# Optimization experiments

Measured on AMD Instinct MI355X. Metric: run time of the kernel, lower is better.

## Reference

```python
import jax, jax.numpy as jnp
import numpy as np

B, S, H, P = 16, 8192, 512, 32

def setup_inputs() -> dict:
    key = jax.random.key(0)
    k1, k2 = jax.random.split(key)
    birnn_outputs = jax.random.normal(k1, (B, S, H), dtype=jnp.float32)
    self_attn = jax.random.normal(k2, (P, H), dtype=jnp.float32)
    return {"birnn_outputs": birnn_outputs, "self_attn": self_attn}

def reference(birnn_outputs, self_attn):
    # scores: [B, P, S] = probes [P,H] x birnn_outputs^T [B,H,S]
    scores = jnp.einsum('ph,bsh->bps', self_attn, birnn_outputs)
    attn = jax.nn.softmax(scores, axis=-1)  # softmax over seq_len
    # context: [B, P, H]
    ctx = jnp.einsum('bps,bsh->bph', attn, birnn_outputs)
    return ctx.reshape(ctx.shape[0], -1)  # [B, P*H]
```

## Files before the change

kernel.cpp:

```cpp
#include <hip/hip_runtime.h>
#include <hip/hip_bf16.h>

#define BB 16
#define SS 8192
#define HH 512
#define PP 32

typedef __attribute__((ext_vector_type(8))) short short8;
typedef __attribute__((ext_vector_type(4))) float f32x4;

__device__ inline unsigned short bf16_hi_trunc(float x) {
  union { float f; unsigned u; } v; v.f = x;
  return (unsigned short)(v.u >> 16);
}
__device__ inline unsigned short bf16_rne(float x) {
  union { float f; unsigned u; } v; v.f = x;
  unsigned r = v.u + 0x7FFFu + ((v.u >> 16) & 1u);
  return (unsigned short)(r >> 16);
}
__device__ inline float from_hi(unsigned short h) {
  union { unsigned u; float f; } v; v.u = ((unsigned)h) << 16;
  return v.f;
}
__device__ inline f32x4 max4(f32x4 a, f32x4 b) {
  f32x4 r; r.x = fmaxf(a.x, b.x); r.y = fmaxf(a.y, b.y);
  r.z = fmaxf(a.z, b.z); r.w = fmaxf(a.w, b.w); return r;
}
__device__ inline f32x4 exp4(f32x4 a) {
  f32x4 r; r.x = __expf(a.x); r.y = __expf(a.y);
  r.z = __expf(a.z); r.w = __expf(a.w); return r;
}
__device__ inline f32x4 fma_b(float a, f32x4 b, f32x4 c) {
  c.x = fmaf(a, b.x, c.x); c.y = fmaf(a, b.y, c.y);
  c.z = fmaf(a, b.z, c.z); c.w = fmaf(a, b.w, c.w); return c;
}
__device__ inline void cvt8(const float* xv, short8& bh, short8& bl) {
#pragma unroll
  for (int j = 0; j < 8; ++j) {
    unsigned short h = bf16_hi_trunc(xv[j]);
    bh[j] = (short)h;
    bl[j] = (short)bf16_rne(xv[j] - from_hi(h));
  }
}

__global__ void k_prep(const float* __restrict__ probes,
                       short* __restrict__ Ph, short* __restrict__ Pl) {
  int t = threadIdx.x;
  for (int q = t; q < 2048; q += 256) {
    int lane = q & 63, kcg = (q >> 6) & 15, nt = q >> 10;
    int p = nt * 16 + (lane & 15);
    int h0 = kcg * 32 + (lane >> 4) * 8;
#pragma unroll
    for (int j = 0; j < 8; ++j) {
      float f = probes[p * HH + h0 + j];
      unsigned short h = bf16_hi_trunc(f);
      Ph[q * 8 + j] = (short)h;
      Pl[q * 8 + j] = (short)bf16_rne(f - from_hi(h));
    }
  }
}

__global__ __launch_bounds__(256) void k_scores4(
    const float* __restrict__ x, const short* __restrict__ Ph,
    const short* __restrict__ Pl, float* __restrict__ scoresT) {
  const int t = threadIdx.x;
  const int lane = t & 63, w = t >> 6;
  const int b = blockIdx.y;
  const int stile = blockIdx.x;

  f32x4 acc[2];
  acc[0] = (f32x4){0.f, 0.f, 0.f, 0.f};
  acc[1] = (f32x4){0.f, 0.f, 0.f, 0.f};

  const int srow = stile * 64 + w * 16 + (lane & 15);
  const float* xr = x + ((size_t)b * SS + srow) * HH + (lane >> 4) * 8;

#pragma unroll 2
  for (int kcg = 0; kcg < 16; ++kcg) {
    f32x4 xa = *(const f32x4*)(xr + kcg * 32);
    f32x4 xc = *(const f32x4*)(xr + kcg * 32 + 4);
    float xv[8] = {xa.x, xa.y, xa.z, xa.w, xc.x, xc.y, xc.z, xc.w};
    short8 xh, xl;
    cvt8(xv, xh, xl);
    short8 ph0 = *(const short8*)(Ph + ((size_t)(kcg * 64 + lane)) * 8);
    short8 pl0 = *(const short8*)(Pl + ((size_t)(kcg * 64 + lane)) * 8);
    short8 ph1 = *(const short8*)(Ph + ((size_t)((16 + kcg) * 64 + lane)) * 8);
    short8 pl1 = *(const short8*)(Pl + ((size_t)((16 + kcg) * 64 + lane)) * 8);
    acc[0] = __builtin_amdgcn_mfma_f32_16x16x32_bf16(xh, ph0, acc[0], 0, 0, 0);
    acc[0] = __builtin_amdgcn_mfma_f32_16x16x32_bf16(xh, pl0, acc[0], 0, 0, 0);
    acc[0] = __builtin_amdgcn_mfma_f32_16x16x32_bf16(xl, ph0, acc[0], 0, 0, 0);
    acc[1] = __builtin_amdgcn_mfma_f32_16x16x32_bf16(xh, ph1, acc[1], 0, 0, 0);
    acc[1] = __builtin_amdgcn_mfma_f32_16x16x32_bf16(xh, pl1, acc[1], 0, 0, 0);
    acc[1] = __builtin_amdgcn_mfma_f32_16x16x32_bf16(xl, ph1, acc[1], 0, 0, 0);
  }

#pragma unroll
  for (int nt = 0; nt < 2; ++nt)
#pragma unroll
    for (int r = 0; r < 4; ++r) {
      int s = stile * 64 + w * 16 + (lane >> 4) * 4 + r;
      int p = nt * 16 + (lane & 15);
      scoresT[((size_t)b * SS + s) * PP + p] = acc[nt][r];
    }
}

__global__ __launch_bounds__(256) void k_stats_a(
    const float* __restrict__ scoresT, float* __restrict__ pm,
    float* __restrict__ pl_) {
  const int blk = blockIdx.x;
  const int b = blk >> 5, sr = blk & 31;
  const int t = threadIdx.x;
  const int p4 = t & 7, sg = t >> 3;
  const f32x4* base = (const f32x4*)(scoresT + ((size_t)b * SS + sr * 256) * PP);

  f32x4 m4 = (f32x4){-1e30f, -1e30f, -1e30f, -1e30f};
  f32x4 l4 = (f32x4){0.f, 0.f, 0.f, 0.f};
#pragma unroll
  for (int i = 0; i < 8; ++i) {
    int s = sg + 32 * i;
    f32x4 v = base[s * 8 + p4];
    f32x4 nm = max4(m4, v);
    l4 = l4 * exp4(m4 - nm) + exp4(v - nm);
    m4 = nm;
  }
  __shared__ f32x4 sm[32][8], sl[32][8];
  sm[sg][p4] = m4;
  sl[sg][p4] = l4;
  __syncthreads();
  if (t < 8) {
    f32x4 M = sm[0][t], L = sl[0][t];
#pragma unroll
    for (int i = 1; i < 32; ++i) {
      f32x4 m2 = sm[i][t], l2 = sl[i][t];
      f32x4 nm = max4(M, m2);
      L = L * exp4(M - nm) + l2 * exp4(m2 - nm);
      M = nm;
    }
    *(f32x4*)&pm[blk * PP + t * 4] = M;
    *(f32x4*)&pl_[blk * PP + t * 4] = L;
  }
}

__global__ __launch_bounds__(256) void k_stats_b(
    const float* __restrict__ pm, const float* __restrict__ pl_,
    float* __restrict__ Mv, float* __restrict__ invl) {
  int i = blockIdx.x * 256 + threadIdx.x;
  if (i >= BB * PP) return;
  int b = i >> 5, p = i & 31;
  float M = -1e30f, L = 0.f;
#pragma unroll
  for (int sr = 0; sr < 32; ++sr) {
    float m2 = pm[(b * 32 + sr) * PP + p], l2 = pl_[(b * 32 + sr) * PP + p];
    float nm = fmaxf(M, m2);
    L = L * __expf(M - nm) + l2 * __expf(m2 - nm);
    M = nm;
  }
  Mv[i] = M;
  invl[i] = 1.0f / L;
}

__global__ __launch_bounds__(256) void k_ctx4(
    const float* __restrict__ x, const float* __restrict__ scoresT,
    const float* __restrict__ Mv, const float* __restrict__ invl,
    float* __restrict__ part) {
  __shared__ float wl[256 * PP];
  const int t = threadIdx.x;
  const int lane = t & 63, w = t >> 6;
  const int sc = blockIdx.x, hh = blockIdx.y, b = blockIdx.z;

  const int pbase = (4 * t) & 31;
  f32x4 mv = *(const f32x4*)(Mv + b * PP + pbase);
  f32x4 il = *(const f32x4*)(invl + b * PP + pbase);
  const f32x4* src = (const f32x4*)(scoresT + ((size_t)b * SS + sc * 256) * PP);
#pragma unroll
  for (int it = 0; it < 8; ++it) {
    f32x4 v = src[t + 256 * it];
    f32x4 e;
    e.x = __expf(v.x - mv.x) * il.x;
    e.y = __expf(v.y - mv.y) * il.y;
    e.z = __expf(v.z - mv.z) * il.z;
    e.w = __expf(v.w - mv.w) * il.w;
    *(f32x4*)&wl[(t + 256 * it) * 4] = e;
  }
  __syncthreads();

  const float* xrow = x + ((size_t)b * SS + sc * 256) * HH + hh * 256 + lane * 4;
  const f32x4* wj = (const f32x4*)wl;

  f32x4 acc[8];
#pragma unroll
  for (int k = 0; k < 8; ++k) acc[k] = (f32x4){0.f, 0.f, 0.f, 0.f};

  for (int jo = 0; jo < 256; jo += 8) {
    f32x4 xv[8];
#pragma unroll
    for (int u = 0; u < 8; ++u)
      xv[u] = *(const f32x4*)(xrow + (size_t)(jo + u) * HH);
#pragma unroll
    for (int u = 0; u < 8; ++u) {
      int j = jo + u;
      f32x4 w0 = wj[j * 8 + w * 2];
      f32x4 w1 = wj[j * 8 + w * 2 + 1];
      acc[0] = fma_b(w0.x, xv[u], acc[0]);
      acc[1] = fma_b(w0.y, xv[u], acc[1]);
      acc[2] = fma_b(w0.z, xv[u], acc[2]);
      acc[3] = fma_b(w0.w, xv[u], acc[3]);
      acc[4] = fma_b(w1.x, xv[u], acc[4]);
      acc[5] = fma_b(w1.y, xv[u], acc[5]);
      acc[6] = fma_b(w1.z, xv[u], acc[6]);
      acc[7] = fma_b(w1.w, xv[u], acc[7]);
    }
  }

#pragma unroll
  for (int pi = 0; pi < 8; ++pi) {
    int p = w * 8 + pi;
    *(f32x4*)(part + (((size_t)sc * BB + b) * PP + p) * HH + hh * 256 + lane * 4) =
        acc[pi];
  }
}

__global__ __launch_bounds__(256) void k_reduce(const float* __restrict__ part,
                                               float* __restrict__ out) {
  int i = blockIdx.x * 256 + threadIdx.x;
  float s = 0.f;
#pragma unroll
  for (int c = 0; c < 32; ++c) s += part[(size_t)c * (BB * PP * HH) + i];
  out[i] = s;
}

extern "C" void kernel_launch(void* const* d_in, const int* in_sizes, int n_in,
                              void* d_out, int out_size, void* d_ws, size_t ws_size,
                              hipStream_t stream) {
  const float* x = (const float*)d_in[0];
  const float* probes = (const float*)d_in[1];
  float* out = (float*)d_out;

  float* scoresT = (float*)d_ws;
  float* part = scoresT + (size_t)BB * SS * PP;
  float* Mv = part + (size_t)32 * BB * PP * HH;
  float* invl = Mv + BB * PP;
  float* pm = invl + BB * PP;
  float* pl_ = pm + 512 * PP;
  short* Ph = (short*)(pl_ + 512 * PP);
  short* Pl = Ph + PP * HH;

  k_prep<<<1, 256, 0, stream>>>(probes, Ph, Pl);
  k_scores4<<<dim3(SS / 64, BB), 256, 0, stream>>>(x, Ph, Pl, scoresT);
  k_stats_a<<<dim3(512), 256, 0, stream>>>(scoresT, pm, pl_);
  k_stats_b<<<dim3(2), 256, 0, stream>>>(pm, pl_, Mv, invl);
  k_ctx4<<<dim3(32, 2, BB), 256, 0, stream>>>(x, scoresT, Mv, invl, part);
  k_reduce<<<dim3(BB * PP * HH / 256), 256, 0, stream>>>(part, out);
}
```

Before: 471.8 us.

## Fuse scores, local softmax and context into one flash-style chunk kernel

```diff
diff --git a/kernel.cpp b/kernel.cpp
--- a/kernel.cpp
+++ b/kernel.cpp
@@ -5,6 +5,8 @@
 #define SS 8192
 #define HH 512
 #define PP 32
+#define NC 32
+#define CH 256
 
 typedef __attribute__((ext_vector_type(8))) short short8;
 typedef __attribute__((ext_vector_type(4))) float f32x4;
@@ -60,173 +62,164 @@
   }
 }
 
-__global__ __launch_bounds__(256) void k_scores4(
+__global__ __launch_bounds__(512, 4) void k_fused(
     const float* __restrict__ x, const short* __restrict__ Ph,
-    const short* __restrict__ Pl, float* __restrict__ scoresT) {
+    const short* __restrict__ Pl, float* __restrict__ pm,
+    float* __restrict__ pl_, float* __restrict__ part) {
+  __shared__ float sc_[CH][36];
+  __shared__ f32x4 sm[64][8];
+  __shared__ f32x4 sl[64][8];
+  __shared__ f32x4 mS4[8];
+
   const int t = threadIdx.x;
   const int lane = t & 63, w = t >> 6;
+  const int scnk = blockIdx.x;
   const int b = blockIdx.y;
-  const int stile = blockIdx.x;
-
-  f32x4 acc[2];
-  acc[0] = (f32x4){0.f, 0.f, 0.f, 0.f};
-  acc[1] = (f32x4){0.f, 0.f, 0.f, 0.f};
-
-  const int srow = stile * 64 + w * 16 + (lane & 15);
-  const float* xr = x + ((size_t)b * SS + srow) * HH + (lane >> 4) * 8;
-
+  const size_t xbase = ((size_t)b * SS + (size_t)scnk * CH) * HH;
+
+#pragma unroll
+  for (int tile = 0; tile < CH / 128; ++tile) {
+    f32x4 acc0 = (f32x4){0.f, 0.f, 0.f, 0.f};
+    f32x4 acc1 = (f32x4){0.f, 0.f, 0.f, 0.f};
+    const int rl = tile * 128 + w * 16 + (lane & 15);
+    const float* xr = x + xbase + (size_t)rl * HH + (lane >> 4) * 8;
 #pragma unroll 2
-  for (int kcg = 0; kcg < 16; ++kcg) {
-    f32x4 xa = *(const f32x4*)(xr + kcg * 32);
-    f32x4 xc = *(const f32x4*)(xr + kcg * 32 + 4);
-    float xv[8] = {xa.x, xa.y, xa.z, xa.w, xc.x, xc.y, xc.z, xc.w};
-    short8 xh, xl;
-    cvt8(xv, xh, xl);
-    short8 ph0 = *(const short8*)(Ph + ((size_t)(kcg * 64 + lane)) * 8);
-    short8 pl0 = *(const short8*)(Pl + ((size_t)(kcg * 64 + lane)) * 8);
-    short8 ph1 = *(const short8*)(Ph + ((size_t)((16 + kcg) * 64 + lane)) * 8);
-    short8 pl1 = *(const short8*)(Pl + ((size_t)((16 + kcg) * 64 + lane)) * 8);
-    acc[0] = __builtin_amdgcn_mfma_f32_16x16x32_bf16(xh, ph0, acc[0], 0, 0, 0);
-    acc[0] = __builtin_amdgcn_mfma_f32_16x16x32_bf16(xh, pl0, acc[0], 0, 0, 0);
-    acc[0] = __builtin_amdgcn_mfma_f32_16x16x32_bf16(xl, ph0, acc[0], 0, 0, 0);
-    acc[1] = __builtin_amdgcn_mfma_f32_16x16x32_bf16(xh, ph1, acc[1], 0, 0, 0);
-    acc[1] = __builtin_amdgcn_mfma_f32_16x16x32_bf16(xh, pl1, acc[1], 0, 0, 0);
-    acc[1] = __builtin_amdgcn_mfma_f32_16x16x32_bf16(xl, ph1, acc[1], 0, 0, 0);
-  }
-
-#pragma unroll
-  for (int nt = 0; nt < 2; ++nt)
+    for (int kcg = 0; kcg < 16; ++kcg) {
+      f32x4 xa = *(const f32x4*)(xr + kcg * 32);
+      f32x4 xc = *(const f32x4*)(xr + kcg * 32 + 4);
+      float xv[8] = {xa.x, xa.y, xa.z, xa.w, xc.x, xc.y, xc.z, xc.w};
+      short8 xh, xl;
+      cvt8(xv, xh, xl);
+      short8 ph0 = *(const short8*)(Ph + ((size_t)(kcg * 64 + lane)) * 8);
+      short8 pl0 = *(const short8*)(Pl + ((size_t)(kcg * 64 + lane)) * 8);
+      short8 ph1 = *(const short8*)(Ph + ((size_t)((16 + kcg) * 64 + lane)) * 8);
+      short8 pl1 = *(const short8*)(Pl + ((size_t)((16 + kcg) * 64 + lane)) * 8);
+      acc0 = __builtin_amdgcn_mfma_f32_16x16x32_bf16(xh, ph0, acc0, 0, 0, 0);
+      acc0 = __builtin_amdgcn_mfma_f32_16x16x32_bf16(xh, pl0, acc0, 0, 0, 0);
+      acc0 = __builtin_amdgcn_mfma_f32_16x16x32_bf16(xl, ph0, acc0, 0, 0, 0);
+      acc1 = __builtin_amdgcn_mfma_f32_16x16x32_bf16(xh, ph1, acc1, 0, 0, 0);
+      acc1 = __builtin_amdgcn_mfma_f32_16x16x32_bf16(xh, pl1, acc1, 0, 0, 0);
+      acc1 = __builtin_amdgcn_mfma_f32_16x16x32_bf16(xl, ph1, acc1, 0, 0, 0);
+    }
 #pragma unroll
     for (int r = 0; r < 4; ++r) {
-      int s = stile * 64 + w * 16 + (lane >> 4) * 4 + r;
-      int p = nt * 16 + (lane & 15);
-      scoresT[((size_t)b * SS + s) * PP + p] = acc[nt][r];
-    }
-}
-
-__global__ __launch_bounds__(256) void k_stats_a(
-    const float* __restrict__ scoresT, float* __restrict__ pm,
-    float* __restrict__ pl_) {
-  const int blk = blockIdx.x;
-  const int b = blk >> 5, sr = blk & 31;
-  const int t = threadIdx.x;
-  const int p4 = t & 7, sg = t >> 3;
-  const f32x4* base = (const f32x4*)(scoresT + ((size_t)b * SS + sr * 256) * PP);
-
-  f32x4 m4 = (f32x4){-1e30f, -1e30f, -1e30f, -1e30f};
-  f32x4 l4 = (f32x4){0.f, 0.f, 0.f, 0.f};
-#pragma unroll
-  for (int i = 0; i < 8; ++i) {
-    int s = sg + 32 * i;
-    f32x4 v = base[s * 8 + p4];
-    f32x4 nm = max4(m4, v);
-    l4 = l4 * exp4(m4 - nm) + exp4(v - nm);
-    m4 = nm;
-  }
-  __shared__ f32x4 sm[32][8], sl[32][8];
-  sm[sg][p4] = m4;
-  sl[sg][p4] = l4;
+      int s_ = tile * 128 + w * 16 + (lane >> 4) * 4 + r;
+      sc_[s_][lane & 15] = acc0[r];
+      sc_[s_][16 + (lane & 15)] = acc1[r];
+    }
+  }
+  __syncthreads();
+
+  {
+    const int p4 = t & 7, sg = t >> 3;
+    f32x4 m4 = (f32x4){-1e30f, -1e30f, -1e30f, -1e30f};
+    f32x4 l4 = (f32x4){0.f, 0.f, 0.f, 0.f};
+#pragma unroll
+    for (int i = 0; i < CH / 64; ++i) {
+      int s_ = sg + 64 * i;
+      f32x4 v = *(const f32x4*)&sc_[s_][p4 * 4];
+      f32x4 nm = max4(m4, v);
+      l4 = l4 * exp4(m4 - nm) + exp4(v - nm);
+      m4 = nm;
+    }
+    sm[sg][p4] = m4;
+    sl[sg][p4] = l4;
+  }
   __syncthreads();
   if (t < 8) {
     f32x4 M = sm[0][t], L = sl[0][t];
 #pragma unroll
-    for (int i = 1; i < 32; ++i) {
+    for (int i = 1; i < 64; ++i) {
       f32x4 m2 = sm[i][t], l2 = sl[i][t];
       f32x4 nm = max4(M, m2);
       L = L * exp4(M - nm) + l2 * exp4(m2 - nm);
       M = nm;
     }
-    *(f32x4*)&pm[blk * PP + t * 4] = M;
-    *(f32x4*)&pl_[blk * PP + t * 4] = L;
-  }
-}
-
-__global__ __launch_bounds__(256) void k_stats_b(
-    const float* __restrict__ pm, const float* __restrict__ pl_,
-    float* __restrict__ Mv, float* __restrict__ invl) {
-  int i = blockIdx.x * 256 + threadIdx.x;
-  if (i >= BB * PP) return;
-  int b = i >> 5, p = i & 31;
-  float M = -1e30f, L = 0.f;
-#pragma unroll
-  for (int sr = 0; sr < 32; ++sr) {
-    float m2 = pm[(b * 32 + sr) * PP + p], l2 = pl_[(b * 32 + sr) * PP + p];
-    float nm = fmaxf(M, m2);
-    L = L * __expf(M - nm) + l2 * __expf(m2 - nm);
-    M = nm;
-  }
-  Mv[i] = M;
-  invl[i] = 1.0f / L;
-}
-
-__global__ __launch_bounds__(256) void k_ctx4(
-    const float* __restrict__ x, const float* __restrict__ scoresT,
-    const float* __restrict__ Mv, const float* __restrict__ invl,
-    float* __restrict__ part) {
-  __shared__ float wl[256 * PP];
+    mS4[t] = M;
+    *(f32x4*)&pm[(size_t)(b * NC + scnk) * PP + t * 4] = M;
+    *(f32x4*)&pl_[(size_t)(b * NC + scnk) * PP + t * 4] = L;
+  }
+  __syncthreads();
+
+  {
+    const float* mSf = (const float*)mS4;
+#pragma unroll
+    for (int i = 0; i < CH * PP / 512; ++i) {
+      int idx = t + 512 * i;
+      int s_ = idx >> 5, p = idx & 31;
+      sc_[s_][p] = __expf(sc_[s_][p] - mSf[p]);
+    }
+  }
+  __syncthreads();
+
+  const float* xrow = x + xbase + lane * 8;
+  f32x4 acc[4][2];
+#pragma unroll
+  for (int pi = 0; pi < 4; ++pi) {
+    acc[pi][0] = (f32x4){0.f, 0.f, 0.f, 0.f};
+    acc[pi][1] = (f32x4){0.f, 0.f, 0.f, 0.f};
+  }
+  for (int jo = 0; jo < CH; jo += 4) {
+    f32x4 xv0[4], xv1[4];
+#pragma unroll
+    for (int u = 0; u < 4; ++u) {
+      const float* xp = xrow + (size_t)(jo + u) * HH;
+      xv0[u] = *(const f32x4*)xp;
+      xv1[u] = *(const f32x4*)(xp + 4);
+    }
+#pragma unroll
+    for (int u = 0; u < 4; ++u) {
+      f32x4 w0 = *(const f32x4*)&sc_[jo + u][w * 4];
+      acc[0][0] = fma_b(w0.x, xv0[u], acc[0][0]);
+      acc[0][1] = fma_b(w0.x, xv1[u], acc[0][1]);
+      acc[1][0] = fma_b(w0.y, xv0[u], acc[1][0]);
+      acc[1][1] = fma_b(w0.y, xv1[u], acc[1][1]);
+      acc[2][0] = fma_b(w0.z, xv0[u], acc[2][0]);
+      acc[2][1] = fma_b(w0.z, xv1[u], acc[2][1]);
+      acc[3][0] = fma_b(w0.w, xv0[u], acc[3][0]);
+      acc[3][1] = fma_b(w0.w, xv1[u], acc[3][1]);
+    }
+  }
+#pragma unroll
+  for (int pi = 0; pi < 4; ++pi) {
+    int p = w * 4 + pi;
+    float* o = part + (((size_t)scnk * BB + b) * PP + p) * HH + lane * 8;
+    *(f32x4*)o = acc[pi][0];
+    *(f32x4*)(o + 4) = acc[pi][1];
+  }
+}
+
+__global__ __launch_bounds__(256) void k_merge(
+    const float* __restrict__ part, const float* __restrict__ pm,
+    const float* __restrict__ pl_, float* __restrict__ out) {
+  const int bp = blockIdx.x;
+  const int b = bp >> 5, p = bp & 31;
   const int t = threadIdx.x;
-  const int lane = t & 63, w = t >> 6;
-  const int sc = blockIdx.x, hh = blockIdx.y, b = blockIdx.z;
-
-  const int pbase = (4 * t) & 31;
-  f32x4 mv = *(const f32x4*)(Mv + b * PP + pbase);
-  f32x4 il = *(const f32x4*)(invl + b * PP + pbase);
-  const f32x4* src = (const f32x4*)(scoresT + ((size_t)b * SS + sc * 256) * PP);
-#pragma unroll
-  for (int it = 0; it < 8; ++it) {
-    f32x4 v = src[t + 256 * it];
-    f32x4 e;
-    e.x = __expf(v.x - mv.x) * il.x;
-    e.y = __expf(v.y - mv.y) * il.y;
-    e.z = __expf(v.z - mv.z) * il.z;
-    e.w = __expf(v.w - mv.w) * il.w;
-    *(f32x4*)&wl[(t + 256 * it) * 4] = e;
-  }
-  __syncthreads();
-
-  const float* xrow = x + ((size_t)b * SS + sc * 256) * HH + hh * 256 + lane * 4;
-  const f32x4* wj = (const f32x4*)wl;
-
-  f32x4 acc[8];
-#pragma unroll
-  for (int k = 0; k < 8; ++k) acc[k] = (f32x4){0.f, 0.f, 0.f, 0.f};
-
-  for (int jo = 0; jo < 256; jo += 8) {
-    f32x4 xv[8];
-#pragma unroll
-    for (int u = 0; u < 8; ++u)
-      xv[u] = *(const f32x4*)(xrow + (size_t)(jo + u) * HH);
-#pragma unroll
-    for (int u = 0; u < 8; ++u) {
-      int j = jo + u;
-      f32x4 w0 = wj[j * 8 + w * 2];
-      f32x4 w1 = wj[j * 8 + w * 2 + 1];
-      acc[0] = fma_b(w0.x, xv[u], acc[0]);
-      acc[1] = fma_b(w0.y, xv[u], acc[1]);
-      acc[2] = fma_b(w0.z, xv[u], acc[2]);
-      acc[3] = fma_b(w0.w, xv[u], acc[3]);
-      acc[4] = fma_b(w1.x, xv[u], acc[4]);
-      acc[5] = fma_b(w1.y, xv[u], acc[5]);
-      acc[6] = fma_b(w1.z, xv[u], acc[6]);
-      acc[7] = fma_b(w1.w, xv[u], acc[7]);
-    }
-  }
-
-#pragma unroll
-  for (int pi = 0; pi < 8; ++pi) {
-    int p = w * 8 + pi;
-    *(f32x4*)(part + (((size_t)sc * BB + b) * PP + p) * HH + hh * 256 + lane * 4) =
-        acc[pi];
-  }
-}
-
-__global__ __launch_bounds__(256) void k_reduce(const float* __restrict__ part,
-                                               float* __restrict__ out) {
-  int i = blockIdx.x * 256 + threadIdx.x;
-  float s = 0.f;
-#pragma unroll
-  for (int c = 0; c < 32; ++c) s += part[(size_t)c * (BB * PP * HH) + i];
-  out[i] = s;
+
+  float M = -1e30f;
+#pragma unroll
+  for (int c = 0; c < NC; ++c)
+    M = fmaxf(M, pm[(size_t)(b * NC + c) * PP + p]);
+  float f[NC];
+  float L = 0.f;
+#pragma unroll
+  for (int c = 0; c < NC; ++c) {
+    float e = __expf(pm[(size_t)(b * NC + c) * PP + p] - M);
+    f[c] = e;
+    L += pl_[(size_t)(b * NC + c) * PP + p] * e;
+  }
+  const float inv = 1.f / L;
+
+  float sx = 0.f, sy = 0.f;
+#pragma unroll
+  for (int c = 0; c < NC; ++c) {
+    const float* q = part + (((size_t)c * BB + b) * PP + p) * HH + t * 2;
+    sx = fmaf(q[0], f[c], sx);
+    sy = fmaf(q[1], f[c], sy);
+  }
+  float* o = out + (size_t)bp * HH + t * 2;
+  o[0] = sx * inv;
+  o[1] = sy * inv;
 }
 
 extern "C" void kernel_launch(void* const* d_in, const int* in_sizes, int n_in,
@@ -236,19 +229,13 @@
   const float* probes = (const float*)d_in[1];
   float* out = (float*)d_out;
 
-  float* scoresT = (float*)d_ws;
-  float* part = scoresT + (size_t)BB * SS * PP;
-  float* Mv = part + (size_t)32 * BB * PP * HH;
-  float* invl = Mv + BB * PP;
-  float* pm = invl + BB * PP;
-  float* pl_ = pm + 512 * PP;
-  short* Ph = (short*)(pl_ + 512 * PP);
+  float* part = (float*)d_ws;
+  float* pm = part + (size_t)NC * BB * PP * HH;
+  float* pl_ = pm + BB * NC * PP;
+  short* Ph = (short*)(pl_ + BB * NC * PP);
   short* Pl = Ph + PP * HH;
 
   k_prep<<<1, 256, 0, stream>>>(probes, Ph, Pl);
-  k_scores4<<<dim3(SS / 64, BB), 256, 0, stream>>>(x, Ph, Pl, scoresT);
-  k_stats_a<<<dim3(512), 256, 0, stream>>>(scoresT, pm, pl_);
-  k_stats_b<<<dim3(2), 256, 0, stream>>>(pm, pl_, Mv, invl);
-  k_ctx4<<<dim3(32, 2, BB), 256, 0, stream>>>(x, scoresT, Mv, invl, part);
-  k_reduce<<<dim3(BB * PP * HH / 256), 256, 0, stream>>>(part, out);
-}
+  k_fused<<<dim3(NC, BB), 512, 0, stream>>>(x, Ph, Pl, pm, pl_, part);
+  k_merge<<<dim3(BB * PP), 256, 0, stream>>>(part, pm, pl_, out);
+}
```

Measured after the change: 483.6 us. 1.02x slower.
